# Performance work log

Measured on AMD Instinct MI355X. Metric: run time of the kernel, lower is better.

## Reference

```python
import jax, jax.numpy as jnp
import numpy as np

N = 32768   # total nodes
E = 524288  # directed edges
F = 128     # input features
H = 128     # hidden width
G = 64      # graphs in batch (N//G = 512 nodes each)


def _lin(key, fan_in, fan_out):
    return jax.random.normal(key, (fan_in, fan_out), jnp.float32) / np.sqrt(fan_in)


def setup_inputs() -> dict:
    key = jax.random.key(0)
    ks = jax.random.split(key, 16)
    d = {}
    d["x"] = jax.random.normal(ks[0], (N, F), jnp.float32)
    d["edge_index"] = jax.random.randint(ks[1], (2, E), 0, N, dtype=jnp.int64)
    d["batch"] = (jnp.arange(N, dtype=jnp.int64) // (N // G))  # sorted, equal-size graphs
    # GCNConv 1 / 2
    d["W1"] = _lin(ks[2], F, H); d["b1"] = jnp.zeros((H,), jnp.float32)
    d["W2"] = _lin(ks[3], H, H); d["b2"] = jnp.zeros((H,), jnp.float32)
    # GraphSelfAttention (per-graph Q/K/V self-attention)
    d["Wq"] = _lin(ks[4], H, H); d["bq"] = jnp.zeros((H,), jnp.float32)
    d["Wk"] = _lin(ks[5], H, H); d["bk"] = jnp.zeros((H,), jnp.float32)
    d["Wv"] = _lin(ks[6], H, H); d["bv"] = jnp.zeros((H,), jnp.float32)
    # MLP head
    d["Wh1"] = _lin(ks[7], H, 64); d["bh1"] = jnp.zeros((64,), jnp.float32)
    d["Wh2"] = _lin(ks[8], 64, 1); d["bh2"] = jnp.zeros((1,), jnp.float32)
    return d


def gcn_conv(x, src, dst, W, b, num_nodes):
    """PyG-style GCNConv: D^{-1/2}(A+I)D^{-1/2} x W + b (self-loops already in src/dst)."""
    h = x @ W                                                    # [N, out]
    deg = jax.ops.segment_sum(jnp.ones_like(dst, dtype=h.dtype), dst,
                              num_segments=num_nodes)            # [N]
    dinv = jax.lax.rsqrt(jnp.maximum(deg, 1.0))
    norm = dinv[src] * dinv[dst]                                 # [E+N]
    msg = h[src] * norm[:, None]                                 # gather
    return jax.ops.segment_sum(msg, dst, num_segments=num_nodes) + b  # scatter-add


def reference(x, edge_index, batch, W1, b1, W2, b2, Wq, bq, Wk, bk, Wv, bv,
              Wh1, bh1, Wh2, bh2):
    num_nodes = x.shape[0]
    loop = jnp.arange(num_nodes, dtype=edge_index.dtype)
    src = jnp.concatenate([edge_index[0], loop])
    dst = jnp.concatenate([edge_index[1], loop])

    x = x.astype(jnp.float32)
    h = jax.nn.relu(gcn_conv(x, src, dst, W1, b1, num_nodes))    # dropout: eval mode (identity)
    h = jax.nn.relu(gcn_conv(h, src, dst, W2, b2, num_nodes))

    # batch = arange // n (equal-size sorted segments) -> dense reshape is exact
    n = num_nodes // G
    hg = h.reshape(G, n, H)                                      # [G, n, H]
    q = hg @ Wq + bq
    k = hg @ Wk + bk
    v = hg @ Wv + bv
    scores = jnp.einsum("gnd,gmd->gnm", q, k) / np.sqrt(H)       # [G, n, n]
    attn = jax.nn.softmax(scores, axis=-1)
    pooled = jnp.einsum("gnm,gmd->gnd", attn, v).mean(axis=1)    # [G, H]

    out = jax.nn.relu(pooled @ Wh1 + bh1) @ Wh2 + bh2            # [G, 1]
    return out
```

## Files before the change

kernel.cpp:

```cpp
#include <hip/hip_runtime.h>
#include <hip/hip_fp16.h>
#include <hip/hip_bf16.h>

#define NN 32768
#define GG 64
#define NPG 512
#define HD 128
#define MAXD 64
#define RSQRT_H 0.08838834764831845f

typedef _Float16 f16;
typedef __attribute__((ext_vector_type(4))) _Float16 f16x4;
typedef __attribute__((ext_vector_type(8))) _Float16 f16x8;
typedef __attribute__((ext_vector_type(4))) float f32x4;

__global__ void k_fill(const int* __restrict__ src, const int* __restrict__ dst,
                       int* __restrict__ cursor, int* __restrict__ ell, int E) {
    int e = blockIdx.x * 256 + threadIdx.x;
    if (e < E) {
        int d = dst[e];
        int slot = atomicAdd(&cursor[d], 1);
        if (slot < MAXD) ell[d * MAXD + slot] = src[e];
    }
}

__global__ void k_wprep(const float* __restrict__ W1, const float* __restrict__ W2,
                        const float* __restrict__ Wq, const float* __restrict__ Wk,
                        f16* __restrict__ wt) {
    const float* Ws[4] = {W1, W2, Wq, Wk};
    int k = blockIdx.x, wsel = blockIdx.y, n = threadIdx.x;
    float v = Ws[wsel][k * HD + n];
    wt[(size_t)wsel * HD * HD + n * HD + k] = (f16)v;
}

template<int AF32, int BIAS>
__global__ __launch_bounds__(256) void k_mgemm(
    const void* __restrict__ Ain, const f16* __restrict__ WT,
    const float* __restrict__ bias, f16* __restrict__ out)
{
    __shared__ f16 Al[64][136];
    __shared__ f16 Wl[128][136];
    int t = threadIdx.x;
    int row0 = blockIdx.x * 64;
    int w = t >> 6, lane = t & 63, lr = lane & 15, lu = lane >> 4;

    if (AF32) {
        const float4* A32 = (const float4*)((const float*)Ain + (size_t)row0 * HD);
#pragma unroll
        for (int i = 0; i < 8; ++i) {
            int idx = t + 256 * i;
            int r = idx >> 5, c4 = idx & 31;
            float4 v = A32[idx];
            f16x4 h = {(f16)v.x, (f16)v.y, (f16)v.z, (f16)v.w};
            *(f16x4*)&Al[r][c4 * 4] = h;
        }
    } else {
        const float4* A16 = (const float4*)((const f16*)Ain + (size_t)row0 * HD);
#pragma unroll
        for (int i = 0; i < 4; ++i) {
            int idx = t + 256 * i;
            int r = idx >> 4, cq = idx & 15;
            *(float4*)&Al[r][cq * 8] = A16[idx];
        }
    }
    const float4* W4 = (const float4*)WT;
#pragma unroll
    for (int i = 0; i < 8; ++i) {
        int idx = t + 256 * i;
        int n = idx >> 4, cq = idx & 15;
        *(float4*)&Wl[n][cq * 8] = W4[idx];
    }
    __syncthreads();

    f16x8 aq[4];
#pragma unroll
    for (int ks = 0; ks < 4; ++ks)
        aq[ks] = *(const f16x8*)&Al[w * 16 + lr][ks * 32 + lu * 8];

    f32x4 acc[8];
#pragma unroll
    for (int ni = 0; ni < 8; ++ni) {
        f32x4 c = {0.f, 0.f, 0.f, 0.f};
#pragma unroll
        for (int ks = 0; ks < 4; ++ks) {
            f16x8 b = *(const f16x8*)&Wl[ni * 16 + lr][ks * 32 + lu * 8];
            c = __builtin_amdgcn_mfma_f32_16x16x32_f16(aq[ks], b, c, 0, 0, 0);
        }
        acc[ni] = c;
    }

    __syncthreads();
#pragma unroll
    for (int ni = 0; ni < 8; ++ni)
#pragma unroll
        for (int j = 0; j < 4; ++j) {
            float v = acc[ni][j];
            if (BIAS) v += bias[ni * 16 + lr];
            Al[w * 16 + lu * 4 + j][ni * 16 + lr] = (f16)v;
        }
    __syncthreads();
    float4* O4 = (float4*)(out + (size_t)row0 * HD);
#pragma unroll
    for (int i = 0; i < 4; ++i) {
        int idx = t + 256 * i;
        int r = idx >> 4, cq = idx & 15;
        O4[idx] = *(float4*)&Al[r][cq * 8];
    }
}

__global__ __launch_bounds__(256) void k_agg(
    const __half* __restrict__ tmat, const int* __restrict__ cursor,
    const int* __restrict__ ell, const float* __restrict__ bias,
    __half* __restrict__ hout)
{
    int t = threadIdx.x;
    int i = blockIdx.x * 4 + (t >> 6);
    int lane = t & 63;
    int cnt = min(cursor[i], MAXD);
    float di = rsqrtf((float)(cnt + 1));
    float2 sv = __half22float2(((const __half2*)(tmat + (size_t)i * HD))[lane]);
    float acc0 = sv.x * (di * di);
    float acc1 = sv.y * (di * di);
    const int* row = ell + (size_t)i * MAXD;
    int e = 0;
    for (; e + 2 <= cnt; e += 2) {
        int s0 = row[e], s1 = row[e + 1];
        float w0 = rsqrtf((float)(min(cursor[s0], MAXD) + 1)) * di;
        float w1 = rsqrtf((float)(min(cursor[s1], MAXD) + 1)) * di;
        float2 v0 = __half22float2(((const __half2*)(tmat + (size_t)s0 * HD))[lane]);
        float2 v1 = __half22float2(((const __half2*)(tmat + (size_t)s1 * HD))[lane]);
        acc0 += v0.x * w0 + v1.x * w1;
        acc1 += v0.y * w0 + v1.y * w1;
    }
    if (e < cnt) {
        int s0 = row[e];
        float w0 = rsqrtf((float)(min(cursor[s0], MAXD) + 1)) * di;
        float2 v0 = __half22float2(((const __half2*)(tmat + (size_t)s0 * HD))[lane]);
        acc0 += v0.x * w0;
        acc1 += v0.y * w0;
    }
    int f = lane * 2;
    __half2 o;
    o.x = __float2half(fmaxf(acc0 + bias[f], 0.f));
    o.y = __float2half(fmaxf(acc1 + bias[f + 1], 0.f));
    ((__half2*)(hout + (size_t)i * HD))[lane] = o;
}

__global__ __launch_bounds__(256, 2) void k_attn(
    const __half* __restrict__ qh,
    const __half* __restrict__ kh,
    float* __restrict__ wpart)
{
    __shared__ f16 Kl[64][136];
    __shared__ float wlp[4][512];
    int t = threadIdx.x;
    int g = blockIdx.x >> 3;
    int qt = blockIdx.x & 7;
    int w = t >> 6, lane = t & 63;
    int lr = lane & 15, lu = lane >> 4;
    int qrow0 = g * NPG + qt * 64;

    f16x8 aq[4];
    {
        const f16* qp = (const f16*)qh + (size_t)(qrow0 + w * 16 + lr) * HD + lu * 8;
#pragma unroll
        for (int ks = 0; ks < 4; ++ks)
            aq[ks] = *(const f16x8*)(qp + ks * 32);
    }

    f32x4 p[8][4];
#pragma unroll
    for (int mt = 0; mt < 8; ++mt) {
        __syncthreads();
        {
            const float4* ks4 = (const float4*)(kh + (size_t)(g * NPG + mt * 64) * HD);
#pragma unroll
            for (int i = 0; i < 4; ++i) {
                int idx = t + 256 * i;
                int row = idx >> 4, cq = idx & 15;
                *(float4*)&Kl[row][cq * 8] = ks4[row * 16 + cq];
            }
        }
        __syncthreads();
#pragma unroll
        for (int ni = 0; ni < 4; ++ni) {
            f32x4 acc = {0.f, 0.f, 0.f, 0.f};
#pragma unroll
            for (int ks = 0; ks < 4; ++ks) {
                f16x8 b = *(const f16x8*)&Kl[ni * 16 + lr][ks * 32 + lu * 8];
                acc = __builtin_amdgcn_mfma_f32_16x16x32_f16(aq[ks], b, acc, 0, 0, 0);
            }
            p[mt][ni] = acc;
        }
    }

    float mrow[4], linv[4];
#pragma unroll
    for (int j = 0; j < 4; ++j) {
        float m = p[0][0][j];
#pragma unroll
        for (int mt = 0; mt < 8; ++mt)
#pragma unroll
            for (int ni = 0; ni < 4; ++ni) m = fmaxf(m, p[mt][ni][j]);
        m = fmaxf(m, __shfl_xor(m, 1));
        m = fmaxf(m, __shfl_xor(m, 2));
        m = fmaxf(m, __shfl_xor(m, 4));
        m = fmaxf(m, __shfl_xor(m, 8));
        mrow[j] = m;
    }
#pragma unroll
    for (int mt = 0; mt < 8; ++mt)
#pragma unroll
        for (int ni = 0; ni < 4; ++ni)
#pragma unroll
            for (int j = 0; j < 4; ++j)
                p[mt][ni][j] = __expf((p[mt][ni][j] - mrow[j]) * RSQRT_H);
#pragma unroll
    for (int j = 0; j < 4; ++j) {
        float l = 0.f;
#pragma unroll
        for (int mt = 0; mt < 8; ++mt)
#pragma unroll
            for (int ni = 0; ni < 4; ++ni) l += p[mt][ni][j];
        l += __shfl_xor(l, 1);
        l += __shfl_xor(l, 2);
        l += __shfl_xor(l, 4);
        l += __shfl_xor(l, 8);
        linv[j] = 1.f / l;
    }
#pragma unroll
    for (int mt = 0; mt < 8; ++mt)
#pragma unroll
        for (int ni = 0; ni < 4; ++ni) {
            float pc = p[mt][ni][0] * linv[0] + p[mt][ni][1] * linv[1]
                     + p[mt][ni][2] * linv[2] + p[mt][ni][3] * linv[3];
            pc += __shfl_xor(pc, 16);
            pc += __shfl_xor(pc, 32);
            if (lu == 0) wlp[w][mt * 64 + ni * 16 + lr] = pc;
        }
    __syncthreads();
    float* wp = wpart + ((size_t)(g * 8 + qt)) * NPG;
    wp[t] = (wlp[0][t] + wlp[1][t] + wlp[2][t] + wlp[3][t]) * (1.f / NPG);
    wp[t + 256] = (wlp[0][t + 256] + wlp[1][t + 256] + wlp[2][t + 256]
                 + wlp[3][t + 256]) * (1.f / NPG);
}

__global__ __launch_bounds__(128) void k_pool(
    const float* __restrict__ wpart, const __half* __restrict__ h,
    float* __restrict__ upart)
{
    __shared__ float wloc[64];
    int b = blockIdx.x;
    int g = b >> 3, ch = b & 7;
    int t = threadIdx.x;
    if (t < 64) {
        float w = 0.f;
#pragma unroll
        for (int qt = 0; qt < 8; ++qt)
            w += wpart[((size_t)(g * 8 + qt)) * NPG + ch * 64 + t];
        wloc[t] = w;
    }
    __syncthreads();
    const __half* hg = h + ((size_t)g * NPG + ch * 64) * HD;
    float u = 0.f;
#pragma unroll 4
    for (int m = 0; m < 64; ++m) u += wloc[m] * __half2float(hg[m * HD + t]);
    upart[(size_t)(ch * GG + g) * HD + t] = u;
}

__global__ __launch_bounds__(128) void k_head2(
    const float* __restrict__ upart,
    const float* __restrict__ Wv, const float* __restrict__ bv,
    const float* __restrict__ Wh1, const float* __restrict__ bh1,
    const float* __restrict__ Wh2, const float* __restrict__ bh2,
    float* __restrict__ out)
{
    __shared__ float ul[128];
    __shared__ float pl[128];
    __shared__ float r1l[64];
    int g = blockIdx.x, t = threadIdx.x;
    float ud = 0.f;
#pragma unroll
    for (int ch = 0; ch < 8; ++ch) ud += upart[(size_t)(ch * GG + g) * HD + t];
    ul[t] = ud;
    __syncthreads();
    float pv = bv[t];
    for (int d = 0; d < HD; ++d) pv += ul[d] * Wv[d * HD + t];
    pl[t] = pv;
    __syncthreads();
    if (t < 64) {
        float r1 = bh1[t];
        for (int d = 0; d < HD; ++d) r1 += pl[d] * Wh1[d * 64 + t];
        r1l[t] = fmaxf(r1, 0.f);
    }
    __syncthreads();
    if (t == 0) {
        float o = bh2[0];
        for (int j = 0; j < 64; ++j) o += r1l[j] * Wh2[j];
        out[g] = o;
    }
}

extern "C" void kernel_launch(void* const* d_in, const int* in_sizes, int n_in,
                              void* d_out, int out_size, void* d_ws, size_t ws_size,
                              hipStream_t stream) {
    const float* x   = (const float*)d_in[0];
    const int* edge  = (const int*)d_in[1];
    const float* W1  = (const float*)d_in[3];
    const float* b1  = (const float*)d_in[4];
    const float* W2  = (const float*)d_in[5];
    const float* b2  = (const float*)d_in[6];
    const float* Wq  = (const float*)d_in[7];
    const float* bq  = (const float*)d_in[8];
    const float* Wk  = (const float*)d_in[9];
    const float* bk  = (const float*)d_in[10];
    const float* Wv  = (const float*)d_in[11];
    const float* bv  = (const float*)d_in[12];
    const float* Wh1 = (const float*)d_in[13];
    const float* bh1 = (const float*)d_in[14];
    const float* Wh2 = (const float*)d_in[15];
    const float* bh2 = (const float*)d_in[16];
    float* out = (float*)d_out;

    int E = in_sizes[1] / 2;
    const int* src = edge;
    const int* dst = edge + E;

    float* tbuf = (float*)d_ws;
    float* hbr  = tbuf + (size_t)NN * HD;
    float* r3   = hbr + (size_t)NN * HD;
    float* wpart = r3 + (size_t)NN * HD;
    int* cursor = (int*)(wpart + GG * 8 * NPG);
    f16* wtb    = (f16*)(cursor + NN);
    __half* tmat = (__half*)tbuf;
    __half* qh   = (__half*)tbuf;
    __half* kh   = qh + (size_t)NN * HD;
    __half* hbuf = (__half*)hbr;
    int* ell    = (int*)r3;
    float* upart = r3;
    f16* W1T = wtb, *W2T = wtb + HD * HD, *WqT = wtb + 2 * HD * HD,
       * WkT = wtb + 3 * HD * HD;

    int eb = (E + 255) / 256;

    hipMemsetAsync(cursor, 0, NN * sizeof(int), stream);
    k_fill<<<eb, 256, 0, stream>>>(src, dst, cursor, ell, E);
    k_wprep<<<dim3(HD, 4), HD, 0, stream>>>(W1, W2, Wq, Wk, wtb);

    k_mgemm<1, 0><<<NN / 64, 256, 0, stream>>>(x, W1T, nullptr, (f16*)tmat);
    k_agg<<<NN / 4, 256, 0, stream>>>(tmat, cursor, ell, b1, hbuf);
    k_mgemm<0, 0><<<NN / 64, 256, 0, stream>>>(hbuf, W2T, nullptr, (f16*)tmat);
    k_agg<<<NN / 4, 256, 0, stream>>>(tmat, cursor, ell, b2, hbuf);
    k_mgemm<0, 1><<<NN / 64, 256, 0, stream>>>(hbuf, WqT, bq, (f16*)qh);
    k_mgemm<0, 1><<<NN / 64, 256, 0, stream>>>(hbuf, WkT, bk, (f16*)kh);
    k_attn<<<GG * 8, 256, 0, stream>>>(qh, kh, wpart);
    k_pool<<<GG * 8, 128, 0, stream>>>(wpart, hbuf, upart);
    k_head2<<<GG, 128, 0, stream>>>(upart, Wv, bv, Wh1, bh1, Wh2, bh2, out);
}
```

Baseline: 262.1 us.

## Double-buffer K tiles in attention, unroll aggregation by four, fuse pool and head

The attention kernel now double-buffers K tiles in shared memory, loading the next tile while MFMAs run on the current one, and drops one barrier per tile. The GCN aggregation loop is unrolled to four neighbours per iteration to keep more gathers in flight. The pool and head kernels are merged into one 64-block kernel, which removes a launch and the upart round trip but leaves only 64 blocks, each reducing over 256 rows. The workspace layout is reshuffled so ell no longer aliases upart.

Measured after the change: 251.4 us. 1.04x faster.

```diff
diff --git a/kernel.cpp b/kernel.cpp
--- a/kernel.cpp
+++ b/kernel.cpp
@@ -59,16 +59,14 @@
 #pragma unroll
         for (int i = 0; i < 4; ++i) {
             int idx = t + 256 * i;
-            int r = idx >> 4, cq = idx & 15;
-            *(float4*)&Al[r][cq * 8] = A16[idx];
+            *(float4*)&Al[idx >> 4][(idx & 15) * 8] = A16[idx];
         }
     }
     const float4* W4 = (const float4*)WT;
 #pragma unroll
     for (int i = 0; i < 8; ++i) {
         int idx = t + 256 * i;
-        int n = idx >> 4, cq = idx & 15;
-        *(float4*)&Wl[n][cq * 8] = W4[idx];
+        *(float4*)&Wl[idx >> 4][(idx & 15) * 8] = W4[idx];
     }
     __syncthreads();
 
@@ -103,8 +101,7 @@
 #pragma unroll
     for (int i = 0; i < 4; ++i) {
         int idx = t + 256 * i;
-        int r = idx >> 4, cq = idx & 15;
-        O4[idx] = *(float4*)&Al[r][cq * 8];
+        O4[idx] = *(float4*)&Al[idx >> 4][(idx & 15) * 8];
     }
 }
 
@@ -123,26 +120,29 @@
     float acc1 = sv.y * (di * di);
     const int* row = ell + (size_t)i * MAXD;
     int e = 0;
-    for (; e + 2 <= cnt; e += 2) {
-        int s0 = row[e], s1 = row[e + 1];
-        float w0 = rsqrtf((float)(min(cursor[s0], MAXD) + 1)) * di;
-        float w1 = rsqrtf((float)(min(cursor[s1], MAXD) + 1)) * di;
+    for (; e + 4 <= cnt; e += 4) {
+        int s0 = row[e], s1 = row[e + 1], s2 = row[e + 2], s3 = row[e + 3];
+        float q0 = rsqrtf((float)(min(cursor[s0], MAXD) + 1)) * di;
+        float q1 = rsqrtf((float)(min(cursor[s1], MAXD) + 1)) * di;
+        float q2 = rsqrtf((float)(min(cursor[s2], MAXD) + 1)) * di;
+        float q3 = rsqrtf((float)(min(cursor[s3], MAXD) + 1)) * di;
         float2 v0 = __half22float2(((const __half2*)(tmat + (size_t)s0 * HD))[lane]);
         float2 v1 = __half22float2(((const __half2*)(tmat + (size_t)s1 * HD))[lane]);
-        acc0 += v0.x * w0 + v1.x * w1;
-        acc1 += v0.y * w0 + v1.y * w1;
-    }
-    if (e < cnt) {
+        float2 v2 = __half22float2(((const __half2*)(tmat + (size_t)s2 * HD))[lane]);
+        float2 v3 = __half22float2(((const __half2*)(tmat + (size_t)s3 * HD))[lane]);
+        acc0 += v0.x * q0 + v1.x * q1 + v2.x * q2 + v3.x * q3;
+        acc1 += v0.y * q0 + v1.y * q1 + v2.y * q2 + v3.y * q3;
+    }
+    for (; e < cnt; ++e) {
         int s0 = row[e];
-        float w0 = rsqrtf((float)(min(cursor[s0], MAXD) + 1)) * di;
+        float q0 = rsqrtf((float)(min(cursor[s0], MAXD) + 1)) * di;
         float2 v0 = __half22float2(((const __half2*)(tmat + (size_t)s0 * HD))[lane]);
-        acc0 += v0.x * w0;
-        acc1 += v0.y * w0;
-    }
-    int f = lane * 2;
+        acc0 += v0.x * q0;
+        acc1 += v0.y * q0;
+    }
     __half2 o;
-    o.x = __float2half(fmaxf(acc0 + bias[f], 0.f));
-    o.y = __float2half(fmaxf(acc1 + bias[f + 1], 0.f));
+    o.x = __float2half(fmaxf(acc0 + bias[lane * 2], 0.f));
+    o.y = __float2half(fmaxf(acc1 + bias[lane * 2 + 1], 0.f));
     ((__half2*)(hout + (size_t)i * HD))[lane] = o;
 }
 
@@ -151,7 +151,7 @@
     const __half* __restrict__ kh,
     float* __restrict__ wpart)
 {
-    __shared__ f16 Kl[64][136];
+    __shared__ f16 Kl[2][64][136];
     __shared__ float wlp[4][512];
     int t = threadIdx.x;
     int g = blockIdx.x >> 3;
@@ -167,27 +167,33 @@
         for (int ks = 0; ks < 4; ++ks)
             aq[ks] = *(const f16x8*)(qp + ks * 32);
     }
+    {
+        const float4* ks4 = (const float4*)(kh + (size_t)(g * NPG) * HD);
+#pragma unroll
+        for (int i = 0; i < 4; ++i) {
+            int idx = t + 256 * i;
+            *(float4*)&Kl[0][idx >> 4][(idx & 15) * 8] = ks4[idx];
+        }
+    }
 
     f32x4 p[8][4];
 #pragma unroll
     for (int mt = 0; mt < 8; ++mt) {
         __syncthreads();
-        {
-            const float4* ks4 = (const float4*)(kh + (size_t)(g * NPG + mt * 64) * HD);
+        if (mt < 7) {
+            const float4* ks4 = (const float4*)(kh + (size_t)(g * NPG + (mt + 1) * 64) * HD);
 #pragma unroll
             for (int i = 0; i < 4; ++i) {
                 int idx = t + 256 * i;
-                int row = idx >> 4, cq = idx & 15;
-                *(float4*)&Kl[row][cq * 8] = ks4[row * 16 + cq];
+                *(float4*)&Kl[(mt + 1) & 1][idx >> 4][(idx & 15) * 8] = ks4[idx];
             }
         }
-        __syncthreads();
 #pragma unroll
         for (int ni = 0; ni < 4; ++ni) {
             f32x4 acc = {0.f, 0.f, 0.f, 0.f};
 #pragma unroll
             for (int ks = 0; ks < 4; ++ks) {
-                f16x8 b = *(const f16x8*)&Kl[ni * 16 + lr][ks * 32 + lu * 8];
+                f16x8 b = *(const f16x8*)&Kl[mt & 1][ni * 16 + lr][ks * 32 + lu * 8];
                 acc = __builtin_amdgcn_mfma_f32_16x16x32_f16(aq[ks], b, acc, 0, 0, 0);
             }
             p[mt][ni] = acc;
@@ -245,48 +251,44 @@
                  + wlp[3][t + 256]) * (1.f / NPG);
 }
 
-__global__ __launch_bounds__(128) void k_pool(
+__global__ __launch_bounds__(256) void k_poolhead(
     const float* __restrict__ wpart, const __half* __restrict__ h,
-    float* __restrict__ upart)
-{
-    __shared__ float wloc[64];
-    int b = blockIdx.x;
-    int g = b >> 3, ch = b & 7;
-    int t = threadIdx.x;
-    if (t < 64) {
-        float w = 0.f;
-#pragma unroll
-        for (int qt = 0; qt < 8; ++qt)
-            w += wpart[((size_t)(g * 8 + qt)) * NPG + ch * 64 + t];
-        wloc[t] = w;
-    }
-    __syncthreads();
-    const __half* hg = h + ((size_t)g * NPG + ch * 64) * HD;
-    float u = 0.f;
-#pragma unroll 4
-    for (int m = 0; m < 64; ++m) u += wloc[m] * __half2float(hg[m * HD + t]);
-    upart[(size_t)(ch * GG + g) * HD + t] = u;
-}
-
-__global__ __launch_bounds__(128) void k_head2(
-    const float* __restrict__ upart,
     const float* __restrict__ Wv, const float* __restrict__ bv,
     const float* __restrict__ Wh1, const float* __restrict__ bh1,
     const float* __restrict__ Wh2, const float* __restrict__ bh2,
     float* __restrict__ out)
 {
+    __shared__ float wloc[512];
+    __shared__ float upar[2][128];
     __shared__ float ul[128];
     __shared__ float pl[128];
     __shared__ float r1l[64];
     int g = blockIdx.x, t = threadIdx.x;
-    float ud = 0.f;
-#pragma unroll
-    for (int ch = 0; ch < 8; ++ch) ud += upart[(size_t)(ch * GG + g) * HD + t];
-    ul[t] = ud;
-    __syncthreads();
-    float pv = bv[t];
-    for (int d = 0; d < HD; ++d) pv += ul[d] * Wv[d * HD + t];
-    pl[t] = pv;
+    {
+        float w0 = 0.f, w1 = 0.f;
+#pragma unroll
+        for (int qt = 0; qt < 8; ++qt) {
+            const float* wp = wpart + ((size_t)(g * 8 + qt)) * NPG;
+            w0 += wp[t]; w1 += wp[t + 256];
+        }
+        wloc[t] = w0; wloc[t + 256] = w1;
+    }
+    __syncthreads();
+    int col = t & 127, half = t >> 7;
+    const __half* hg = h + ((size_t)g * NPG + half * 256) * HD;
+    float u = 0.f;
+#pragma unroll 4
+    for (int m = 0; m < 256; ++m)
+        u += wloc[half * 256 + m] * __half2float(hg[(size_t)m * HD + col]);
+    upar[half][col] = u;
+    __syncthreads();
+    if (t < 128) ul[t] = upar[0][t] + upar[1][t];
+    __syncthreads();
+    if (t < 128) {
+        float pv = bv[t];
+        for (int d = 0; d < HD; ++d) pv += ul[d] * Wv[d * HD + t];
+        pl[t] = pv;
+    }
     __syncthreads();
     if (t < 64) {
         float r1 = bh1[t];
@@ -326,18 +328,14 @@
     const int* src = edge;
     const int* dst = edge + E;
 
-    float* tbuf = (float*)d_ws;
-    float* hbr  = tbuf + (size_t)NN * HD;
-    float* r3   = hbr + (size_t)NN * HD;
-    float* wpart = r3 + (size_t)NN * HD;
+    f16* tmat = (f16*)d_ws;
+    f16* qh   = tmat;
+    f16* kh   = qh + (size_t)NN * HD;
+    __half* hbuf = (__half*)(kh + (size_t)NN * HD);
+    int* ell = (int*)((f16*)hbuf + 2 * (size_t)NN * HD);
+    float* wpart = (float*)(ell + (size_t)NN * MAXD);
     int* cursor = (int*)(wpart + GG * 8 * NPG);
     f16* wtb    = (f16*)(cursor + NN);
-    __half* tmat = (__half*)tbuf;
-    __half* qh   = (__half*)tbuf;
-    __half* kh   = qh + (size_t)NN * HD;
-    __half* hbuf = (__half*)hbr;
-    int* ell    = (int*)r3;
-    float* upart = r3;
     f16* W1T = wtb, *W2T = wtb + HD * HD, *WqT = wtb + 2 * HD * HD,
        * WkT = wtb + 3 * HD * HD;
 
@@ -347,13 +345,12 @@
     k_fill<<<eb, 256, 0, stream>>>(src, dst, cursor, ell, E);
     k_wprep<<<dim3(HD, 4), HD, 0, stream>>>(W1, W2, Wq, Wk, wtb);
 
-    k_mgemm<1, 0><<<NN / 64, 256, 0, stream>>>(x, W1T, nullptr, (f16*)tmat);
-    k_agg<<<NN / 4, 256, 0, stream>>>(tmat, cursor, ell, b1, hbuf);
-    k_mgemm<0, 0><<<NN / 64, 256, 0, stream>>>(hbuf, W2T, nullptr, (f16*)tmat);
-    k_agg<<<NN / 4, 256, 0, stream>>>(tmat, cursor, ell, b2, hbuf);
-    k_mgemm<0, 1><<<NN / 64, 256, 0, stream>>>(hbuf, WqT, bq, (f16*)qh);
-    k_mgemm<0, 1><<<NN / 64, 256, 0, stream>>>(hbuf, WkT, bk, (f16*)kh);
-    k_attn<<<GG * 8, 256, 0, stream>>>(qh, kh, wpart);
-    k_pool<<<GG * 8, 128, 0, stream>>>(wpart, hbuf, upart);
-    k_head2<<<GG, 128, 0, stream>>>(upart, Wv, bv, Wh1, bh1, Wh2, bh2, out);
-}
+    k_mgemm<1, 0><<<NN / 64, 256, 0, stream>>>(x, W1T, nullptr, tmat);
+    k_agg<<<NN / 4, 256, 0, stream>>>((const __half*)tmat, cursor, ell, b1, hbuf);
+    k_mgemm<0, 0><<<NN / 64, 256, 0, stream>>>(hbuf, W2T, nullptr, tmat);
+    k_agg<<<NN / 4, 256, 0, stream>>>((const __half*)tmat, cursor, ell, b2, hbuf);
+    k_mgemm<0, 1><<<NN / 64, 256, 0, stream>>>(hbuf, WqT, bq, qh);
+    k_mgemm<0, 1><<<NN / 64, 256, 0, stream>>>(hbuf, WkT, bk, kh);
+    k_attn<<<GG * 8, 256, 0, stream>>>((const __half*)qh, (const __half*)kh, wpart);
+    k_poolhead<<<GG, 256, 0, stream>>>(wpart, hbuf, Wv, bv, Wh1, bh1, Wh2, bh2, out);
+}
```
